# Kernel tuning notes

Hardware: AMD Instinct MI355X
Metric: run time of the kernel (lower is better)

## Reference

```python
import jax, jax.numpy as jnp
import numpy as np

N, E, D, C = 50000, 800000, 96, 40
L2_EPS = 1e-12  # tf.nn.l2_normalize epsilon


def setup_inputs() -> dict:
    key = jax.random.key(0)
    ks = jax.random.split(key, 8)
    row = jnp.sort(jax.random.randint(ks[0], (E,), 0, N, dtype=jnp.int32))
    col = jax.random.randint(ks[1], (E,), 0, N, dtype=jnp.int32)
    vals = jax.random.uniform(ks[2], (E,), dtype=jnp.float32)
    x = jax.random.normal(ks[3], (N, D), dtype=jnp.float32)
    w1 = jax.random.normal(ks[4], (D, D), dtype=jnp.float32) * 0.1
    w2 = jax.random.normal(ks[5], (D, D), dtype=jnp.float32) * 0.1
    wc = jax.random.normal(ks[6], (D, C), dtype=jnp.float32) * 0.1
    bc = jnp.zeros((C,), dtype=jnp.float32)
    return {"row": row, "col": col, "vals": vals, "x": x,
            "w1": w1, "w2": w2, "wc": wc, "bc": bc}


def _spmm(row, col, vals, h):
    # sparse A (coo: row, col, vals) @ dense h, via gather + segment_sum
    msg = vals[:, None] * h[col]            # [E, D]
    return jax.ops.segment_sum(msg, row, num_segments=N)


def reference(row, col, vals, x, w1, w2, wc, bc):
    h = x
    for w in (w1, w2):                       # GCNConv: act(A @ (h @ W)), no bias
        h = jax.nn.relu(_spmm(row, col, vals, h @ w))
    # tf.nn.l2_normalize(h, axis=1)
    sq = jnp.sum(h * h, axis=1, keepdims=True)
    out = h * jax.lax.rsqrt(jnp.maximum(sq, L2_EPS))
    probs = jax.nn.softmax(out @ wc + bc, axis=-1)
    return out, probs
```

## Files before the change

kernel.cpp:

```cpp
#include <hip/hip_runtime.h>
#include <hip/hip_bf16.h>

#define GN 50000
#define GE 800000
#define GD 96
#define GC 40
#define L2EPS 1e-12f

typedef __attribute__((ext_vector_type(8))) short short8v;
typedef __attribute__((ext_vector_type(4))) float f32x4;

__device__ __forceinline__ unsigned f2bf(float x) {
    union { float f; unsigned u; } v; v.f = x;
    return (v.u + 0x7fffu + ((v.u >> 16) & 1u)) >> 16;
}
__device__ __forceinline__ float bflo(unsigned u) { return __uint_as_float(u << 16); }
__device__ __forceinline__ float bfhi(unsigned u) { return __uint_as_float(u & 0xffff0000u); }

__global__ void prep_k(const int* __restrict__ row, const int* __restrict__ col,
                       const float* __restrict__ vals, int* __restrict__ rp,
                       int2* __restrict__ ep) {
    int i = blockIdx.x * blockDim.x + threadIdx.x;
    if (i < GE) ep[i] = make_int2(col[i], __float_as_int(vals[i]));
    if (i <= GN) {
        int lo = 0, hi = GE;
        while (lo < hi) {
            int mid = (lo + hi) >> 1;
            if (row[mid] < i) lo = mid + 1; else hi = mid;
        }
        rp[i] = lo;
    }
}

__global__ void wpack_k(const float* __restrict__ w1, const float* __restrict__ w2,
                        unsigned* __restrict__ Wb1, unsigned* __restrict__ Wb2) {
    int idx = blockIdx.x * blockDim.x + threadIdx.x;
    if (idx >= 2 * 4608) return;
    const float* W = (idx < 4608) ? w1 : w2;
    unsigned* Wb   = (idx < 4608) ? Wb1 : Wb2;
    int i = (idx < 4608) ? idx : idx - 4608;
    int r = i & 3;
    int lane = (i >> 2) & 63;
    int frag = i >> 8;
    int nt = frag / 3, kt = frag - nt * 3;
    int col = nt * 16 + (lane & 15);
    int k = kt * 32 + (lane >> 4) * 8 + r * 2;
    Wb[i] = f2bf(W[k * GD + col]) | (f2bf(W[(k + 1) * GD + col]) << 16);
}

__global__ __launch_bounds__(64) void gemm_mfma_k(const float* __restrict__ A,
                                                  const uint4* __restrict__ Wb,
                                                  unsigned short* __restrict__ O) {
    const int tile = blockIdx.x;
    const int l  = threadIdx.x;
    const int m  = l & 15;
    const int kg = l >> 4;

    const float* arow = A + (size_t)(tile * 16 + m) * GD + kg * 8;
    short8v ah[3], al[3];
#pragma unroll
    for (int kt = 0; kt < 3; ++kt) {
        const float4* ap = reinterpret_cast<const float4*>(arow + kt * 32);
        float4 x0 = ap[0], x1 = ap[1];
        uint4 H, L;
        H.x = f2bf(x0.x) | (f2bf(x0.y) << 16);
        H.y = f2bf(x0.z) | (f2bf(x0.w) << 16);
        H.z = f2bf(x1.x) | (f2bf(x1.y) << 16);
        H.w = f2bf(x1.z) | (f2bf(x1.w) << 16);
        L.x = f2bf(x0.x - bflo(H.x)) | (f2bf(x0.y - bfhi(H.x)) << 16);
        L.y = f2bf(x0.z - bflo(H.y)) | (f2bf(x0.w - bfhi(H.y)) << 16);
        L.z = f2bf(x1.x - bflo(H.z)) | (f2bf(x1.y - bfhi(H.z)) << 16);
        L.w = f2bf(x1.z - bflo(H.w)) | (f2bf(x1.w - bfhi(H.w)) << 16);
        union { uint4 u; short8v s; } ch, cl;
        ch.u = H; cl.u = L;
        ah[kt] = ch.s; al[kt] = cl.s;
    }

#pragma unroll
    for (int nt = 0; nt < 6; ++nt) {
        f32x4 acc = {0.f, 0.f, 0.f, 0.f};
#pragma unroll
        for (int kt = 0; kt < 3; ++kt) {
            union { uint4 u; short8v s; } b;
            b.u = Wb[(nt * 3 + kt) * 64 + l];
            acc = __builtin_amdgcn_mfma_f32_16x16x32_bf16(ah[kt], b.s, acc, 0, 0, 0);
            acc = __builtin_amdgcn_mfma_f32_16x16x32_bf16(al[kt], b.s, acc, 0, 0, 0);
        }
        int ccol = nt * 16 + m;
#pragma unroll
        for (int reg = 0; reg < 4; ++reg) {
            int rrow = tile * 16 + kg * 4 + reg;
            O[(size_t)rrow * GD + ccol] = (unsigned short)f2bf(acc[reg]);
        }
    }
}

#define SPMM_BODY(POST)                                                              \
    int idx = blockIdx.x * blockDim.x + threadIdx.x;                                 \
    int n = idx >> 3;                                                                \
    int t = idx & 7;                                                                 \
    if (n >= GN) return;                                                             \
    int e0 = rp[n], e1 = rp[n + 1];                                                  \
    const unsigned* base = Tb;                                                       \
    float a0=0,a1=0,a2=0,a3=0,a4=0,a5=0,a6=0,a7=0,a8=0,a9=0,a10=0,a11=0;             \
    _Pragma("unroll 2")                                                              \
    for (int e = e0; e < e1; ++e) {                                                  \
        int2 p = ep[e];                                                              \
        float v = __int_as_float(p.y);                                               \
        const unsigned* r = base + (size_t)p.x * 48;                                 \
        uint4 u = *reinterpret_cast<const uint4*>(r + t * 4);                        \
        uint2 w = *reinterpret_cast<const uint2*>(r + 32 + t * 2);                   \
        a0 += v * bflo(u.x); a1 += v * bfhi(u.x);                                    \
        a2 += v * bflo(u.y); a3 += v * bfhi(u.y);                                    \
        a4 += v * bflo(u.z); a5 += v * bfhi(u.z);                                    \
        a6 += v * bflo(u.w); a7 += v * bfhi(u.w);                                    \
        a8 += v * bflo(w.x); a9 += v * bfhi(w.x);                                    \
        a10 += v * bflo(w.y); a11 += v * bfhi(w.y);                                  \
    }                                                                                \
    a0=fmaxf(a0,0.f); a1=fmaxf(a1,0.f); a2=fmaxf(a2,0.f); a3=fmaxf(a3,0.f);          \
    a4=fmaxf(a4,0.f); a5=fmaxf(a5,0.f); a6=fmaxf(a6,0.f); a7=fmaxf(a7,0.f);          \
    a8=fmaxf(a8,0.f); a9=fmaxf(a9,0.f); a10=fmaxf(a10,0.f); a11=fmaxf(a11,0.f);      \
    POST                                                                             \
    float4* hr = reinterpret_cast<float4*>(H + (size_t)n * GD + t * 8);              \
    hr[0] = make_float4(a0, a1, a2, a3);                                             \
    hr[1] = make_float4(a4, a5, a6, a7);                                             \
    *reinterpret_cast<float4*>(H + (size_t)n * GD + 64 + t * 4) =                    \
        make_float4(a8, a9, a10, a11);

__global__ void spmm_relu_k(const int* __restrict__ rp, const int2* __restrict__ ep,
                            const unsigned* __restrict__ Tb, float* __restrict__ H) {
    SPMM_BODY(;)
}

__global__ void spmm_relu_norm_k(const int* __restrict__ rp, const int2* __restrict__ ep,
                                 const unsigned* __restrict__ Tb, float* __restrict__ H) {
    SPMM_BODY(
        float ss = a0*a0+a1*a1+a2*a2+a3*a3+a4*a4+a5*a5+a6*a6+a7*a7+a8*a8+a9*a9+a10*a10+a11*a11;
        ss += __shfl_xor(ss, 1);
        ss += __shfl_xor(ss, 2);
        ss += __shfl_xor(ss, 4);
        float s = rsqrtf(fmaxf(ss, L2EPS));
        a0*=s; a1*=s; a2*=s; a3*=s; a4*=s; a5*=s;
        a6*=s; a7*=s; a8*=s; a9*=s; a10*=s; a11*=s;
    )
}

__global__ void cls_gemm_k(const float* __restrict__ A, const float* __restrict__ WC,
                           const float* __restrict__ BC, float* __restrict__ L) {
    __shared__ float4 w4[GD * 10];
    const float4* W4 = reinterpret_cast<const float4*>(WC);
    for (int i = threadIdx.x; i < GD * 10; i += blockDim.x) w4[i] = W4[i];
    __syncthreads();
    int idx = blockIdx.x * blockDim.x + threadIdx.x;
    if (idx >= (GN / 4) * 10) return;
    int rq = idx / 10;
    int q  = idx - rq * 10;
    int r0 = rq * 4;
    const float* a = A + (size_t)r0 * GD;
    float4 acc0 = {0,0,0,0}, acc1 = {0,0,0,0}, acc2 = {0,0,0,0}, acc3 = {0,0,0,0};
    for (int k0 = 0; k0 < GD; k0 += 4) {
        float4 a0 = *reinterpret_cast<const float4*>(a + k0);
        float4 a1 = *reinterpret_cast<const float4*>(a + GD + k0);
        float4 a2 = *reinterpret_cast<const float4*>(a + 2 * GD + k0);
        float4 a3 = *reinterpret_cast<const float4*>(a + 3 * GD + k0);
#pragma unroll
        for (int kk = 0; kk < 4; ++kk) {
            float4 w = w4[(k0 + kk) * 10 + q];
            float s0 = ((const float*)&a0)[kk];
            float s1 = ((const float*)&a1)[kk];
            float s2 = ((const float*)&a2)[kk];
            float s3 = ((const float*)&a3)[kk];
            acc0.x += s0 * w.x; acc0.y += s0 * w.y; acc0.z += s0 * w.z; acc0.w += s0 * w.w;
            acc1.x += s1 * w.x; acc1.y += s1 * w.y; acc1.z += s1 * w.z; acc1.w += s1 * w.w;
            acc2.x += s2 * w.x; acc2.y += s2 * w.y; acc2.z += s2 * w.z; acc2.w += s2 * w.w;
            acc3.x += s3 * w.x; acc3.y += s3 * w.y; acc3.z += s3 * w.z; acc3.w += s3 * w.w;
        }
    }
    float4 b = *reinterpret_cast<const float4*>(BC + q * 4);
    acc0.x += b.x; acc0.y += b.y; acc0.z += b.z; acc0.w += b.w;
    acc1.x += b.x; acc1.y += b.y; acc1.z += b.z; acc1.w += b.w;
    acc2.x += b.x; acc2.y += b.y; acc2.z += b.z; acc2.w += b.w;
    acc3.x += b.x; acc3.y += b.y; acc3.z += b.z; acc3.w += b.w;
    float4* L4 = reinterpret_cast<float4*>(L);
    L4[(size_t)(r0 + 0) * 10 + q] = acc0;
    L4[(size_t)(r0 + 1) * 10 + q] = acc1;
    L4[(size_t)(r0 + 2) * 10 + q] = acc2;
    L4[(size_t)(r0 + 3) * 10 + q] = acc3;
}

__global__ void softmax_k(const float* __restrict__ L, float* __restrict__ PROBS) {
    int n = blockIdx.x * blockDim.x + threadIdx.x;
    if (n >= GN) return;
    const float4* lr = reinterpret_cast<const float4*>(L + (size_t)n * GC);
    float4 v[10];
#pragma unroll
    for (int i = 0; i < 10; ++i) v[i] = lr[i];
    float m = -1e30f;
#pragma unroll
    for (int i = 0; i < 10; ++i)
        m = fmaxf(m, fmaxf(fmaxf(v[i].x, v[i].y), fmaxf(v[i].z, v[i].w)));
    float sum = 0.f;
#pragma unroll
    for (int i = 0; i < 10; ++i) {
        v[i].x = __expf(v[i].x - m); v[i].y = __expf(v[i].y - m);
        v[i].z = __expf(v[i].z - m); v[i].w = __expf(v[i].w - m);
        sum += v[i].x + v[i].y + v[i].z + v[i].w;
    }
    float inv = 1.f / sum;
    float4* pr = reinterpret_cast<float4*>(PROBS + (size_t)n * GC);
#pragma unroll
    for (int i = 0; i < 10; ++i) {
        v[i].x *= inv; v[i].y *= inv; v[i].z *= inv; v[i].w *= inv;
        pr[i] = v[i];
    }
}

extern "C" void kernel_launch(void* const* d_in, const int* in_sizes, int n_in,
                              void* d_out, int out_size, void* d_ws, size_t ws_size,
                              hipStream_t stream) {
    const int*   row  = (const int*)d_in[0];
    const int*   col  = (const int*)d_in[1];
    const float* vals = (const float*)d_in[2];
    const float* x    = (const float*)d_in[3];
    const float* w1   = (const float*)d_in[4];
    const float* w2   = (const float*)d_in[5];
    const float* wc   = (const float*)d_in[6];
    const float* bc   = (const float*)d_in[7];

    float* out   = (float*)d_out;
    float* probs = out + (size_t)GN * GD;

    char*  ws  = (char*)d_ws;
    int*   rp  = (int*)ws;
    size_t off = (((size_t)(GN + 1) * 4) + 511) & ~(size_t)511;
    unsigned* buf = (unsigned*)(ws + off);
    off += (size_t)GN * GD * 4;
    off = (off + 511) & ~(size_t)511;
    int2* ep   = (int2*)(ws + off);
    off += (size_t)GE * 8;
    off = (off + 511) & ~(size_t)511;
    unsigned* Wb1 = (unsigned*)(ws + off);
    unsigned* Wb2 = Wb1 + 4608;

    prep_k<<<(GE + 255) / 256, 256, 0, stream>>>(row, col, vals, rp, ep);
    wpack_k<<<(2 * 4608 + 255) / 256, 256, 0, stream>>>(w1, w2, Wb1, Wb2);
    gemm_mfma_k<<<GN / 16, 64, 0, stream>>>(x, (const uint4*)Wb1, (unsigned short*)buf);
    spmm_relu_k<<<(GN * 8 + 255) / 256, 256, 0, stream>>>(rp, ep, buf, out);
    gemm_mfma_k<<<GN / 16, 64, 0, stream>>>(out, (const uint4*)Wb2, (unsigned short*)buf);
    spmm_relu_norm_k<<<(GN * 8 + 255) / 256, 256, 0, stream>>>(rp, ep, buf, out);
    cls_gemm_k<<<((GN / 4) * 10 + 255) / 256, 256, 0, stream>>>(out, wc, bc, (float*)buf);
    softmax_k<<<(GN + 255) / 256, 256, 0, stream>>>((float*)buf, probs);
}
```

Baseline: 113.3 us.

## Fuse second SpMM with L2 norm, classifier and softmax; merge weight packing into prep

Merges the weight packing kernel into the CSR prep kernel. The second SpMM now computes the L2 normalisation, the classifier GEMM (with weights staged in LDS) and the softmax in one block-level kernel, so the logits no longer round-trip through global memory and three launches become one. Both SpMM kernels switch to 12 threads per row, each loading one 16-byte chunk instead of a 16-byte plus an 8-byte load. The cost is heavy LDS use (about 15KB of classifier weights per 192-thread block) and several block barriers, plus 2 of every 12 threads idle during the classifier and softmax.

Result: faster. 108.3 us (-4.4%).

```diff
diff --git a/kernel.cpp b/kernel.cpp
--- a/kernel.cpp
+++ b/kernel.cpp
@@ -18,8 +18,10 @@
 __device__ __forceinline__ float bfhi(unsigned u) { return __uint_as_float(u & 0xffff0000u); }
 
 __global__ void prep_k(const int* __restrict__ row, const int* __restrict__ col,
-                       const float* __restrict__ vals, int* __restrict__ rp,
-                       int2* __restrict__ ep) {
+                       const float* __restrict__ vals, const float* __restrict__ w1,
+                       const float* __restrict__ w2, int* __restrict__ rp,
+                       int2* __restrict__ ep, unsigned* __restrict__ Wb1,
+                       unsigned* __restrict__ Wb2) {
     int i = blockIdx.x * blockDim.x + threadIdx.x;
     if (i < GE) ep[i] = make_int2(col[i], __float_as_int(vals[i]));
     if (i <= GN) {
@@ -30,22 +32,18 @@
         }
         rp[i] = lo;
     }
-}
-
-__global__ void wpack_k(const float* __restrict__ w1, const float* __restrict__ w2,
-                        unsigned* __restrict__ Wb1, unsigned* __restrict__ Wb2) {
-    int idx = blockIdx.x * blockDim.x + threadIdx.x;
-    if (idx >= 2 * 4608) return;
-    const float* W = (idx < 4608) ? w1 : w2;
-    unsigned* Wb   = (idx < 4608) ? Wb1 : Wb2;
-    int i = (idx < 4608) ? idx : idx - 4608;
-    int r = i & 3;
-    int lane = (i >> 2) & 63;
-    int frag = i >> 8;
-    int nt = frag / 3, kt = frag - nt * 3;
-    int col = nt * 16 + (lane & 15);
-    int k = kt * 32 + (lane >> 4) * 8 + r * 2;
-    Wb[i] = f2bf(W[k * GD + col]) | (f2bf(W[(k + 1) * GD + col]) << 16);
+    if (i < 2 * 4608) {
+        const float* W = (i < 4608) ? w1 : w2;
+        unsigned* Wb   = (i < 4608) ? Wb1 : Wb2;
+        int j = (i < 4608) ? i : i - 4608;
+        int r = j & 3;
+        int lane = (j >> 2) & 63;
+        int frag = j >> 8;
+        int nt = frag / 3, kt = frag - nt * 3;
+        int c = nt * 16 + (lane & 15);
+        int k = kt * 32 + (lane >> 4) * 8 + r * 2;
+        Wb[j] = f2bf(W[k * GD + c]) | (f2bf(W[(k + 1) * GD + c]) << 16);
+    }
 }
 
 __global__ __launch_bounds__(64) void gemm_mfma_k(const float* __restrict__ A,
@@ -95,123 +93,107 @@
     }
 }
 
-#define SPMM_BODY(POST)                                                              \
-    int idx = blockIdx.x * blockDim.x + threadIdx.x;                                 \
-    int n = idx >> 3;                                                                \
-    int t = idx & 7;                                                                 \
-    if (n >= GN) return;                                                             \
-    int e0 = rp[n], e1 = rp[n + 1];                                                  \
-    const unsigned* base = Tb;                                                       \
-    float a0=0,a1=0,a2=0,a3=0,a4=0,a5=0,a6=0,a7=0,a8=0,a9=0,a10=0,a11=0;             \
-    _Pragma("unroll 2")                                                              \
-    for (int e = e0; e < e1; ++e) {                                                  \
-        int2 p = ep[e];                                                              \
-        float v = __int_as_float(p.y);                                               \
-        const unsigned* r = base + (size_t)p.x * 48;                                 \
-        uint4 u = *reinterpret_cast<const uint4*>(r + t * 4);                        \
-        uint2 w = *reinterpret_cast<const uint2*>(r + 32 + t * 2);                   \
-        a0 += v * bflo(u.x); a1 += v * bfhi(u.x);                                    \
-        a2 += v * bflo(u.y); a3 += v * bfhi(u.y);                                    \
-        a4 += v * bflo(u.z); a5 += v * bfhi(u.z);                                    \
-        a6 += v * bflo(u.w); a7 += v * bfhi(u.w);                                    \
-        a8 += v * bflo(w.x); a9 += v * bfhi(w.x);                                    \
-        a10 += v * bflo(w.y); a11 += v * bfhi(w.y);                                  \
-    }                                                                                \
-    a0=fmaxf(a0,0.f); a1=fmaxf(a1,0.f); a2=fmaxf(a2,0.f); a3=fmaxf(a3,0.f);          \
-    a4=fmaxf(a4,0.f); a5=fmaxf(a5,0.f); a6=fmaxf(a6,0.f); a7=fmaxf(a7,0.f);          \
-    a8=fmaxf(a8,0.f); a9=fmaxf(a9,0.f); a10=fmaxf(a10,0.f); a11=fmaxf(a11,0.f);      \
-    POST                                                                             \
-    float4* hr = reinterpret_cast<float4*>(H + (size_t)n * GD + t * 8);              \
-    hr[0] = make_float4(a0, a1, a2, a3);                                             \
-    hr[1] = make_float4(a4, a5, a6, a7);                                             \
-    *reinterpret_cast<float4*>(H + (size_t)n * GD + 64 + t * 4) =                    \
-        make_float4(a8, a9, a10, a11);
-
 __global__ void spmm_relu_k(const int* __restrict__ rp, const int2* __restrict__ ep,
                             const unsigned* __restrict__ Tb, float* __restrict__ H) {
-    SPMM_BODY(;)
-}
-
-__global__ void spmm_relu_norm_k(const int* __restrict__ rp, const int2* __restrict__ ep,
-                                 const unsigned* __restrict__ Tb, float* __restrict__ H) {
-    SPMM_BODY(
-        float ss = a0*a0+a1*a1+a2*a2+a3*a3+a4*a4+a5*a5+a6*a6+a7*a7+a8*a8+a9*a9+a10*a10+a11*a11;
-        ss += __shfl_xor(ss, 1);
-        ss += __shfl_xor(ss, 2);
-        ss += __shfl_xor(ss, 4);
-        float s = rsqrtf(fmaxf(ss, L2EPS));
-        a0*=s; a1*=s; a2*=s; a3*=s; a4*=s; a5*=s;
-        a6*=s; a7*=s; a8*=s; a9*=s; a10*=s; a11*=s;
-    )
-}
-
-__global__ void cls_gemm_k(const float* __restrict__ A, const float* __restrict__ WC,
-                           const float* __restrict__ BC, float* __restrict__ L) {
-    __shared__ float4 w4[GD * 10];
-    const float4* W4 = reinterpret_cast<const float4*>(WC);
-    for (int i = threadIdx.x; i < GD * 10; i += blockDim.x) w4[i] = W4[i];
-    __syncthreads();
     int idx = blockIdx.x * blockDim.x + threadIdx.x;
-    if (idx >= (GN / 4) * 10) return;
-    int rq = idx / 10;
-    int q  = idx - rq * 10;
-    int r0 = rq * 4;
-    const float* a = A + (size_t)r0 * GD;
-    float4 acc0 = {0,0,0,0}, acc1 = {0,0,0,0}, acc2 = {0,0,0,0}, acc3 = {0,0,0,0};
-    for (int k0 = 0; k0 < GD; k0 += 4) {
-        float4 a0 = *reinterpret_cast<const float4*>(a + k0);
-        float4 a1 = *reinterpret_cast<const float4*>(a + GD + k0);
-        float4 a2 = *reinterpret_cast<const float4*>(a + 2 * GD + k0);
-        float4 a3 = *reinterpret_cast<const float4*>(a + 3 * GD + k0);
-#pragma unroll
-        for (int kk = 0; kk < 4; ++kk) {
-            float4 w = w4[(k0 + kk) * 10 + q];
-            float s0 = ((const float*)&a0)[kk];
-            float s1 = ((const float*)&a1)[kk];
-            float s2 = ((const float*)&a2)[kk];
-            float s3 = ((const float*)&a3)[kk];
-            acc0.x += s0 * w.x; acc0.y += s0 * w.y; acc0.z += s0 * w.z; acc0.w += s0 * w.w;
-            acc1.x += s1 * w.x; acc1.y += s1 * w.y; acc1.z += s1 * w.z; acc1.w += s1 * w.w;
-            acc2.x += s2 * w.x; acc2.y += s2 * w.y; acc2.z += s2 * w.z; acc2.w += s2 * w.w;
-            acc3.x += s3 * w.x; acc3.y += s3 * w.y; acc3.z += s3 * w.z; acc3.w += s3 * w.w;
-        }
-    }
-    float4 b = *reinterpret_cast<const float4*>(BC + q * 4);
-    acc0.x += b.x; acc0.y += b.y; acc0.z += b.z; acc0.w += b.w;
-    acc1.x += b.x; acc1.y += b.y; acc1.z += b.z; acc1.w += b.w;
-    acc2.x += b.x; acc2.y += b.y; acc2.z += b.z; acc2.w += b.w;
-    acc3.x += b.x; acc3.y += b.y; acc3.z += b.z; acc3.w += b.w;
-    float4* L4 = reinterpret_cast<float4*>(L);
-    L4[(size_t)(r0 + 0) * 10 + q] = acc0;
-    L4[(size_t)(r0 + 1) * 10 + q] = acc1;
-    L4[(size_t)(r0 + 2) * 10 + q] = acc2;
-    L4[(size_t)(r0 + 3) * 10 + q] = acc3;
-}
-
-__global__ void softmax_k(const float* __restrict__ L, float* __restrict__ PROBS) {
-    int n = blockIdx.x * blockDim.x + threadIdx.x;
+    int n = idx / 12;
     if (n >= GN) return;
-    const float4* lr = reinterpret_cast<const float4*>(L + (size_t)n * GC);
-    float4 v[10];
-#pragma unroll
-    for (int i = 0; i < 10; ++i) v[i] = lr[i];
-    float m = -1e30f;
-#pragma unroll
-    for (int i = 0; i < 10; ++i)
-        m = fmaxf(m, fmaxf(fmaxf(v[i].x, v[i].y), fmaxf(v[i].z, v[i].w)));
-    float sum = 0.f;
-#pragma unroll
-    for (int i = 0; i < 10; ++i) {
-        v[i].x = __expf(v[i].x - m); v[i].y = __expf(v[i].y - m);
-        v[i].z = __expf(v[i].z - m); v[i].w = __expf(v[i].w - m);
-        sum += v[i].x + v[i].y + v[i].z + v[i].w;
-    }
-    float inv = 1.f / sum;
-    float4* pr = reinterpret_cast<float4*>(PROBS + (size_t)n * GC);
-#pragma unroll
-    for (int i = 0; i < 10; ++i) {
-        v[i].x *= inv; v[i].y *= inv; v[i].z *= inv; v[i].w *= inv;
-        pr[i] = v[i];
+    int t = idx - n * 12;
+    int e0 = rp[n], e1 = rp[n + 1];
+    float a0=0,a1=0,a2=0,a3=0,a4=0,a5=0,a6=0,a7=0;
+#pragma unroll 2
+    for (int e = e0; e < e1; ++e) {
+        int2 p = ep[e];
+        float v = __int_as_float(p.y);
+        uint4 u = *reinterpret_cast<const uint4*>(Tb + (size_t)p.x * 48 + t * 4);
+        a0 += v * bflo(u.x); a1 += v * bfhi(u.x);
+        a2 += v * bflo(u.y); a3 += v * bfhi(u.y);
+        a4 += v * bflo(u.z); a5 += v * bfhi(u.z);
+        a6 += v * bflo(u.w); a7 += v * bfhi(u.w);
+    }
+    float4* hr = reinterpret_cast<float4*>(H + (size_t)n * GD + t * 8);
+    hr[0] = make_float4(fmaxf(a0,0.f), fmaxf(a1,0.f), fmaxf(a2,0.f), fmaxf(a3,0.f));
+    hr[1] = make_float4(fmaxf(a4,0.f), fmaxf(a5,0.f), fmaxf(a6,0.f), fmaxf(a7,0.f));
+}
+
+__global__ __launch_bounds__(192) void spmm_norm_cls_k(
+        const int* __restrict__ rp, const int2* __restrict__ ep,
+        const unsigned* __restrict__ Tb, const float* __restrict__ WC,
+        const float* __restrict__ BC, float* __restrict__ H,
+        float* __restrict__ PROBS) {
+    __shared__ float  wlds[GD * GC];
+    __shared__ float  sq[192];
+    __shared__ float  srow[16][100];
+    __shared__ float  smax[16][10];
+    __shared__ float  selse[16][GC];
+
+    const int tid = threadIdx.x;
+    {
+        float4* w4 = reinterpret_cast<float4*>(wlds);
+        const float4* W4 = reinterpret_cast<const float4*>(WC);
+        for (int i = tid; i < GD * GC / 4; i += 192) w4[i] = W4[i];
+    }
+    const int g = tid / 12;
+    const int t = tid - g * 12;
+    const int n = blockIdx.x * 16 + g;
+    int e0 = rp[n], e1 = rp[n + 1];
+    float a0=0,a1=0,a2=0,a3=0,a4=0,a5=0,a6=0,a7=0;
+#pragma unroll 2
+    for (int e = e0; e < e1; ++e) {
+        int2 p = ep[e];
+        float v = __int_as_float(p.y);
+        uint4 u = *reinterpret_cast<const uint4*>(Tb + (size_t)p.x * 48 + t * 4);
+        a0 += v * bflo(u.x); a1 += v * bfhi(u.x);
+        a2 += v * bflo(u.y); a3 += v * bfhi(u.y);
+        a4 += v * bflo(u.z); a5 += v * bfhi(u.z);
+        a6 += v * bflo(u.w); a7 += v * bfhi(u.w);
+    }
+    a0=fmaxf(a0,0.f); a1=fmaxf(a1,0.f); a2=fmaxf(a2,0.f); a3=fmaxf(a3,0.f);
+    a4=fmaxf(a4,0.f); a5=fmaxf(a5,0.f); a6=fmaxf(a6,0.f); a7=fmaxf(a7,0.f);
+    sq[tid] = a0*a0+a1*a1+a2*a2+a3*a3+a4*a4+a5*a5+a6*a6+a7*a7;
+    __syncthreads();
+    float s2 = 0.f;
+#pragma unroll
+    for (int j = 0; j < 12; ++j) s2 += sq[g * 12 + j];
+    float s = rsqrtf(fmaxf(s2, L2EPS));
+    a0*=s; a1*=s; a2*=s; a3*=s; a4*=s; a5*=s; a6*=s; a7*=s;
+    float4* hr = reinterpret_cast<float4*>(H + (size_t)n * GD + t * 8);
+    hr[0] = make_float4(a0, a1, a2, a3);
+    hr[1] = make_float4(a4, a5, a6, a7);
+    float* sr = &srow[g][t * 8];
+    sr[0]=a0; sr[1]=a1; sr[2]=a2; sr[3]=a3; sr[4]=a4; sr[5]=a5; sr[6]=a6; sr[7]=a7;
+    __syncthreads();
+
+    float4 acc = {0.f, 0.f, 0.f, 0.f};
+    if (t < 10) {
+        const float4* wl4 = reinterpret_cast<const float4*>(wlds);
+        const float* row = srow[g];
+        acc = *reinterpret_cast<const float4*>(BC + t * 4);
+#pragma unroll 8
+        for (int k = 0; k < GD; ++k) {
+            float sv = row[k];
+            float4 w = wl4[k * 10 + t];
+            acc.x += sv * w.x; acc.y += sv * w.y; acc.z += sv * w.z; acc.w += sv * w.w;
+        }
+        smax[g][t] = fmaxf(fmaxf(acc.x, acc.y), fmaxf(acc.z, acc.w));
+    }
+    __syncthreads();
+    if (t < 10) {
+        float m = smax[g][0];
+#pragma unroll
+        for (int j = 1; j < 10; ++j) m = fmaxf(m, smax[g][j]);
+        acc.x = __expf(acc.x - m); acc.y = __expf(acc.y - m);
+        acc.z = __expf(acc.z - m); acc.w = __expf(acc.w - m);
+        *reinterpret_cast<float4*>(&selse[g][t * 4]) = acc;
+    }
+    __syncthreads();
+    if (t < 10) {
+        float sum = 0.f;
+#pragma unroll
+        for (int j = 0; j < GC; ++j) sum += selse[g][j];
+        float inv = 1.f / sum;
+        acc.x *= inv; acc.y *= inv; acc.z *= inv; acc.w *= inv;
+        *reinterpret_cast<float4*>(PROBS + (size_t)n * GC + t * 4) = acc;
     }
 }
 
@@ -242,12 +224,9 @@
     unsigned* Wb1 = (unsigned*)(ws + off);
     unsigned* Wb2 = Wb1 + 4608;
 
-    prep_k<<<(GE + 255) / 256, 256, 0, stream>>>(row, col, vals, rp, ep);
-    wpack_k<<<(2 * 4608 + 255) / 256, 256, 0, stream>>>(w1, w2, Wb1, Wb2);
+    prep_k<<<(GE + 255) / 256, 256, 0, stream>>>(row, col, vals, w1, w2, rp, ep, Wb1, Wb2);
     gemm_mfma_k<<<GN / 16, 64, 0, stream>>>(x, (const uint4*)Wb1, (unsigned short*)buf);
-    spmm_relu_k<<<(GN * 8 + 255) / 256, 256, 0, stream>>>(rp, ep, buf, out);
+    spmm_relu_k<<<(GN * 12 + 255) / 256, 256, 0, stream>>>(rp, ep, buf, out);
     gemm_mfma_k<<<GN / 16, 64, 0, stream>>>(out, (const uint4*)Wb2, (unsigned short*)buf);
-    spmm_relu_norm_k<<<(GN * 8 + 255) / 256, 256, 0, stream>>>(rp, ep, buf, out);
-    cls_gemm_k<<<((GN / 4) * 10 + 255) / 256, 256, 0, stream>>>(out, wc, bc, (float*)buf);
-    softmax_k<<<(GN + 255) / 256, 256, 0, stream>>>((float*)buf, probs);
-}
+    spmm_norm_cls_k<<<GN / 16, 192, 0, stream>>>(rp, ep, buf, wc, bc, out, probs);
+}
```

## Drop edge-pair packing, fuse weight packing into prep, unroll SpMM gathers

Applied to the files above, without the earlier changes.

Removes the packed (col,val) edge array and reads the col and vals inputs directly in both SpMM kernels, so the prep kernel no longer touches all edges. The weight bf16 packing kernel is merged into prep_k, saving one launch. The first SpMM switches to 12 threads per node, each handling 8 features with a single 16-byte gather. Both SpMM loops are manually unrolled by 4 to keep more independent gathers in flight. The trade-off is two separate index and value loads per edge instead of one 8-byte load, plus non-power-of-two thread indexing in the first SpMM.

Result: faster. 108.9 us (-3.8%).

```diff
diff --git a/kernel.cpp b/kernel.cpp
--- a/kernel.cpp
+++ b/kernel.cpp
@@ -17,11 +17,10 @@
 __device__ __forceinline__ float bflo(unsigned u) { return __uint_as_float(u << 16); }
 __device__ __forceinline__ float bfhi(unsigned u) { return __uint_as_float(u & 0xffff0000u); }
 
-__global__ void prep_k(const int* __restrict__ row, const int* __restrict__ col,
-                       const float* __restrict__ vals, int* __restrict__ rp,
-                       int2* __restrict__ ep) {
+__global__ void prep_k(const int* __restrict__ row, const float* __restrict__ w1,
+                       const float* __restrict__ w2, int* __restrict__ rp,
+                       unsigned* __restrict__ Wb1, unsigned* __restrict__ Wb2) {
     int i = blockIdx.x * blockDim.x + threadIdx.x;
-    if (i < GE) ep[i] = make_int2(col[i], __float_as_int(vals[i]));
     if (i <= GN) {
         int lo = 0, hi = GE;
         while (lo < hi) {
@@ -30,22 +29,18 @@
         }
         rp[i] = lo;
     }
-}
-
-__global__ void wpack_k(const float* __restrict__ w1, const float* __restrict__ w2,
-                        unsigned* __restrict__ Wb1, unsigned* __restrict__ Wb2) {
-    int idx = blockIdx.x * blockDim.x + threadIdx.x;
-    if (idx >= 2 * 4608) return;
-    const float* W = (idx < 4608) ? w1 : w2;
-    unsigned* Wb   = (idx < 4608) ? Wb1 : Wb2;
-    int i = (idx < 4608) ? idx : idx - 4608;
-    int r = i & 3;
-    int lane = (i >> 2) & 63;
-    int frag = i >> 8;
-    int nt = frag / 3, kt = frag - nt * 3;
-    int col = nt * 16 + (lane & 15);
-    int k = kt * 32 + (lane >> 4) * 8 + r * 2;
-    Wb[i] = f2bf(W[k * GD + col]) | (f2bf(W[(k + 1) * GD + col]) << 16);
+    if (i < 2 * 4608) {
+        const float* W = (i < 4608) ? w1 : w2;
+        unsigned* Wb   = (i < 4608) ? Wb1 : Wb2;
+        int j = (i < 4608) ? i : i - 4608;
+        int r = j & 3;
+        int lane = (j >> 2) & 63;
+        int frag = j >> 8;
+        int nt = frag / 3, kt = frag - nt * 3;
+        int c = nt * 16 + (lane & 15);
+        int k = kt * 32 + (lane >> 4) * 8 + r * 2;
+        Wb[j] = f2bf(W[k * GD + c]) | (f2bf(W[(k + 1) * GD + c]) << 16);
+    }
 }
 
 __global__ __launch_bounds__(64) void gemm_mfma_k(const float* __restrict__ A,
@@ -95,54 +90,98 @@
     }
 }
 
-#define SPMM_BODY(POST)                                                              \
-    int idx = blockIdx.x * blockDim.x + threadIdx.x;                                 \
-    int n = idx >> 3;                                                                \
-    int t = idx & 7;                                                                 \
-    if (n >= GN) return;                                                             \
-    int e0 = rp[n], e1 = rp[n + 1];                                                  \
-    const unsigned* base = Tb;                                                       \
-    float a0=0,a1=0,a2=0,a3=0,a4=0,a5=0,a6=0,a7=0,a8=0,a9=0,a10=0,a11=0;             \
-    _Pragma("unroll 2")                                                              \
-    for (int e = e0; e < e1; ++e) {                                                  \
-        int2 p = ep[e];                                                              \
-        float v = __int_as_float(p.y);                                               \
-        const unsigned* r = base + (size_t)p.x * 48;                                 \
-        uint4 u = *reinterpret_cast<const uint4*>(r + t * 4);                        \
-        uint2 w = *reinterpret_cast<const uint2*>(r + 32 + t * 2);                   \
-        a0 += v * bflo(u.x); a1 += v * bfhi(u.x);                                    \
-        a2 += v * bflo(u.y); a3 += v * bfhi(u.y);                                    \
-        a4 += v * bflo(u.z); a5 += v * bfhi(u.z);                                    \
-        a6 += v * bflo(u.w); a7 += v * bfhi(u.w);                                    \
-        a8 += v * bflo(w.x); a9 += v * bfhi(w.x);                                    \
-        a10 += v * bflo(w.y); a11 += v * bfhi(w.y);                                  \
-    }                                                                                \
-    a0=fmaxf(a0,0.f); a1=fmaxf(a1,0.f); a2=fmaxf(a2,0.f); a3=fmaxf(a3,0.f);          \
-    a4=fmaxf(a4,0.f); a5=fmaxf(a5,0.f); a6=fmaxf(a6,0.f); a7=fmaxf(a7,0.f);          \
-    a8=fmaxf(a8,0.f); a9=fmaxf(a9,0.f); a10=fmaxf(a10,0.f); a11=fmaxf(a11,0.f);      \
-    POST                                                                             \
-    float4* hr = reinterpret_cast<float4*>(H + (size_t)n * GD + t * 8);              \
-    hr[0] = make_float4(a0, a1, a2, a3);                                             \
-    hr[1] = make_float4(a4, a5, a6, a7);                                             \
-    *reinterpret_cast<float4*>(H + (size_t)n * GD + 64 + t * 4) =                    \
+#define FMA8(U, V)                                                    \
+    a0 += (V) * bflo((U).x); a1 += (V) * bfhi((U).x);                 \
+    a2 += (V) * bflo((U).y); a3 += (V) * bfhi((U).y);                 \
+    a4 += (V) * bflo((U).z); a5 += (V) * bfhi((U).z);                 \
+    a6 += (V) * bflo((U).w); a7 += (V) * bfhi((U).w);
+
+__global__ void spmm_relu_k(const int* __restrict__ rp, const int* __restrict__ col,
+                            const float* __restrict__ vals,
+                            const unsigned* __restrict__ Tb, float* __restrict__ H) {
+    int idx = blockIdx.x * blockDim.x + threadIdx.x;
+    int n = idx / 12;
+    if (n >= GN) return;
+    int t = idx - n * 12;
+    int e0 = rp[n], e1 = rp[n + 1];
+    float a0=0,a1=0,a2=0,a3=0,a4=0,a5=0,a6=0,a7=0;
+    int e = e0;
+    for (; e + 4 <= e1; e += 4) {
+        int c0 = col[e], c1 = col[e+1], c2 = col[e+2], c3 = col[e+3];
+        float v0 = vals[e], v1 = vals[e+1], v2 = vals[e+2], v3 = vals[e+3];
+        uint4 u0 = *reinterpret_cast<const uint4*>(Tb + (size_t)c0 * 48 + t * 4);
+        uint4 u1 = *reinterpret_cast<const uint4*>(Tb + (size_t)c1 * 48 + t * 4);
+        uint4 u2 = *reinterpret_cast<const uint4*>(Tb + (size_t)c2 * 48 + t * 4);
+        uint4 u3 = *reinterpret_cast<const uint4*>(Tb + (size_t)c3 * 48 + t * 4);
+        FMA8(u0, v0) FMA8(u1, v1) FMA8(u2, v2) FMA8(u3, v3)
+    }
+    for (; e < e1; ++e) {
+        float v = vals[e];
+        uint4 u = *reinterpret_cast<const uint4*>(Tb + (size_t)col[e] * 48 + t * 4);
+        FMA8(u, v)
+    }
+    float4* hr = reinterpret_cast<float4*>(H + (size_t)n * GD + t * 8);
+    hr[0] = make_float4(fmaxf(a0,0.f), fmaxf(a1,0.f), fmaxf(a2,0.f), fmaxf(a3,0.f));
+    hr[1] = make_float4(fmaxf(a4,0.f), fmaxf(a5,0.f), fmaxf(a6,0.f), fmaxf(a7,0.f));
+}
+
+#define FMA12(U, W_, V)                                               \
+    a0 += (V) * bflo((U).x); a1 += (V) * bfhi((U).x);                 \
+    a2 += (V) * bflo((U).y); a3 += (V) * bfhi((U).y);                 \
+    a4 += (V) * bflo((U).z); a5 += (V) * bfhi((U).z);                 \
+    a6 += (V) * bflo((U).w); a7 += (V) * bfhi((U).w);                 \
+    a8 += (V) * bflo((W_).x); a9 += (V) * bfhi((W_).x);               \
+    a10 += (V) * bflo((W_).y); a11 += (V) * bfhi((W_).y);
+
+__global__ void spmm_relu_norm_k(const int* __restrict__ rp, const int* __restrict__ col,
+                                 const float* __restrict__ vals,
+                                 const unsigned* __restrict__ Tb, float* __restrict__ H) {
+    int idx = blockIdx.x * blockDim.x + threadIdx.x;
+    int n = idx >> 3;
+    if (n >= GN) return;
+    int t = idx & 7;
+    int e0 = rp[n], e1 = rp[n + 1];
+    float a0=0,a1=0,a2=0,a3=0,a4=0,a5=0,a6=0,a7=0,a8=0,a9=0,a10=0,a11=0;
+    int e = e0;
+    for (; e + 4 <= e1; e += 4) {
+        int c0 = col[e], c1 = col[e+1], c2 = col[e+2], c3 = col[e+3];
+        float v0 = vals[e], v1 = vals[e+1], v2 = vals[e+2], v3 = vals[e+3];
+        const unsigned* r0p = Tb + (size_t)c0 * 48;
+        const unsigned* r1p = Tb + (size_t)c1 * 48;
+        const unsigned* r2p = Tb + (size_t)c2 * 48;
+        const unsigned* r3p = Tb + (size_t)c3 * 48;
+        uint4 u0 = *reinterpret_cast<const uint4*>(r0p + t * 4);
+        uint2 w0 = *reinterpret_cast<const uint2*>(r0p + 32 + t * 2);
+        uint4 u1 = *reinterpret_cast<const uint4*>(r1p + t * 4);
+        uint2 w1 = *reinterpret_cast<const uint2*>(r1p + 32 + t * 2);
+        uint4 u2 = *reinterpret_cast<const uint4*>(r2p + t * 4);
+        uint2 w2 = *reinterpret_cast<const uint2*>(r2p + 32 + t * 2);
+        uint4 u3 = *reinterpret_cast<const uint4*>(r3p + t * 4);
+        uint2 w3 = *reinterpret_cast<const uint2*>(r3p + 32 + t * 2);
+        FMA12(u0, w0, v0) FMA12(u1, w1, v1) FMA12(u2, w2, v2) FMA12(u3, w3, v3)
+    }
+    for (; e < e1; ++e) {
+        float v = vals[e];
+        const unsigned* r = Tb + (size_t)col[e] * 48;
+        uint4 u = *reinterpret_cast<const uint4*>(r + t * 4);
+        uint2 w = *reinterpret_cast<const uint2*>(r + 32 + t * 2);
+        FMA12(u, w, v)
+    }
+    a0=fmaxf(a0,0.f); a1=fmaxf(a1,0.f); a2=fmaxf(a2,0.f); a3=fmaxf(a3,0.f);
+    a4=fmaxf(a4,0.f); a5=fmaxf(a5,0.f); a6=fmaxf(a6,0.f); a7=fmaxf(a7,0.f);
+    a8=fmaxf(a8,0.f); a9=fmaxf(a9,0.f); a10=fmaxf(a10,0.f); a11=fmaxf(a11,0.f);
+    float ss = a0*a0+a1*a1+a2*a2+a3*a3+a4*a4+a5*a5+a6*a6+a7*a7+a8*a8+a9*a9+a10*a10+a11*a11;
+    ss += __shfl_xor(ss, 1);
+    ss += __shfl_xor(ss, 2);
+    ss += __shfl_xor(ss, 4);
+    float s = rsqrtf(fmaxf(ss, L2EPS));
+    a0*=s; a1*=s; a2*=s; a3*=s; a4*=s; a5*=s;
+    a6*=s; a7*=s; a8*=s; a9*=s; a10*=s; a11*=s;
+    float4* hr = reinterpret_cast<float4*>(H + (size_t)n * GD + t * 8);
+    hr[0] = make_float4(a0, a1, a2, a3);
+    hr[1] = make_float4(a4, a5, a6, a7);
+    *reinterpret_cast<float4*>(H + (size_t)n * GD + 64 + t * 4) =
         make_float4(a8, a9, a10, a11);
-
-__global__ void spmm_relu_k(const int* __restrict__ rp, const int2* __restrict__ ep,
-                            const unsigned* __restrict__ Tb, float* __restrict__ H) {
-    SPMM_BODY(;)
-}
-
-__global__ void spmm_relu_norm_k(const int* __restrict__ rp, const int2* __restrict__ ep,
-                                 const unsigned* __restrict__ Tb, float* __restrict__ H) {
-    SPMM_BODY(
-        float ss = a0*a0+a1*a1+a2*a2+a3*a3+a4*a4+a5*a5+a6*a6+a7*a7+a8*a8+a9*a9+a10*a10+a11*a11;
-        ss += __shfl_xor(ss, 1);
-        ss += __shfl_xor(ss, 2);
-        ss += __shfl_xor(ss, 4);
-        float s = rsqrtf(fmaxf(ss, L2EPS));
-        a0*=s; a1*=s; a2*=s; a3*=s; a4*=s; a5*=s;
-        a6*=s; a7*=s; a8*=s; a9*=s; a10*=s; a11*=s;
-    )
 }
 
 __global__ void cls_gemm_k(const float* __restrict__ A, const float* __restrict__ WC,
@@ -236,18 +275,14 @@
     unsigned* buf = (unsigned*)(ws + off);
     off += (size_t)GN * GD * 4;
     off = (off + 511) & ~(size_t)511;
-    int2* ep   = (int2*)(ws + off);
-    off += (size_t)GE * 8;
-    off = (off + 511) & ~(size_t)511;
     unsigned* Wb1 = (unsigned*)(ws + off);
     unsigned* Wb2 = Wb1 + 4608;
 
-    prep_k<<<(GE + 255) / 256, 256, 0, stream>>>(row, col, vals, rp, ep);
-    wpack_k<<<(2 * 4608 + 255) / 256, 256, 0, stream>>>(w1, w2, Wb1, Wb2);
+    prep_k<<<(GN + 1 + 255) / 256, 256, 0, stream>>>(row, w1, w2, rp, Wb1, Wb2);
     gemm_mfma_k<<<GN / 16, 64, 0, stream>>>(x, (const uint4*)Wb1, (unsigned short*)buf);
-    spmm_relu_k<<<(GN * 8 + 255) / 256, 256, 0, stream>>>(rp, ep, buf, out);
+    spmm_relu_k<<<(GN * 12 + 255) / 256, 256, 0, stream>>>(rp, col, vals, buf, out);
     gemm_mfma_k<<<GN / 16, 64, 0, stream>>>(out, (const uint4*)Wb2, (unsigned short*)buf);
-    spmm_relu_norm_k<<<(GN * 8 + 255) / 256, 256, 0, stream>>>(rp, ep, buf, out);
+    spmm_relu_norm_k<<<(GN * 8 + 255) / 256, 256, 0, stream>>>(rp, col, vals, buf, out);
     cls_gemm_k<<<((GN / 4) * 10 + 255) / 256, 256, 0, stream>>>(out, wc, bc, (float*)buf);
     softmax_k<<<(GN + 255) / 256, 256, 0, stream>>>((float*)buf, probs);
 }
```
